# Kernel tuning notes

Measured on AMD Instinct MI355X. Metric: run time of the kernel, lower is better.

## Reference

```python
import jax, jax.numpy as jnp
import numpy as np

EMBED_DIM = 1024
N_HEAD = 16
HEAD_DIM = EMBED_DIM // N_HEAD


def setup_inputs() -> dict:
    key = jax.random.key(0)
    k1, k2, k3 = jax.random.split(key, 3)
    B, S = 2, 2048
    x = jax.random.normal(k1, (B, S, EMBED_DIM), dtype=jnp.float32)
    # kaiming-style scale for the packed QKV projection and output projection
    w_qkv = jax.random.normal(k2, (3 * EMBED_DIM, EMBED_DIM), dtype=jnp.float32) * np.sqrt(2.0 / EMBED_DIM)
    w0 = jax.random.normal(k3, (EMBED_DIM, EMBED_DIM), dtype=jnp.float32) * np.sqrt(2.0 / EMBED_DIM)
    return {"x": x, "w_qkv": w_qkv, "w0": w0}


def reference(x, w_qkv, w0):
    B, S, E = x.shape
    # fused QKV projection (Linear with no bias): x @ w_qkv.T -> [B,S,3E]
    qkv = jnp.einsum('bse,fe->bsf', x, w_qkv)
    q, k, v = jnp.split(qkv, 3, axis=-1)
    # reshape to [B, H, S, D]
    def heads(t):
        return t.reshape(B, S, N_HEAD, HEAD_DIM).transpose(0, 2, 1, 3)
    q, k, v = heads(q), heads(k), heads(v)
    scale = 1.0 / np.sqrt(HEAD_DIM).astype(np.float32)
    scores = jnp.einsum('bhsd,bhtd->bhst', q, k) * scale  # [B,H,S,S]
    # causal additive bias: -inf above the diagonal (same math as the precomputed bias tensor)
    causal = jnp.tril(jnp.ones((S, S), dtype=bool))
    scores = jnp.where(causal, scores, -jnp.inf)
    probs = jax.nn.softmax(scores, axis=-1)
    e = jnp.einsum('bhst,bhtd->bhsd', probs, v)  # [B,H,S,D]
    e = e.transpose(0, 2, 1, 3).reshape(B, S, E)
    # output projection: E @ w0.T
    return jnp.einsum('bse,fe->bsf', e, w0)
```

## Files before the change

### kernel.cpp

```cpp
#include <hip/hip_runtime.h>


typedef unsigned short u16;
typedef short bf16x8 __attribute__((ext_vector_type(8)));
typedef float f32x4 __attribute__((ext_vector_type(4)));
typedef unsigned short u16x4 __attribute__((ext_vector_type(4)));

#define S_LEN 2048
#define EMB 1024
#define NH 16
#define HD 64
#define QKV_W 3072
#define BATCH 2
#define CSC 0.18033688f
#define PSTR 72

static __device__ __forceinline__ u16 f2bf(float f) {
    unsigned x = __float_as_uint(f);
    return (u16)((x + 0x7fffu + ((x >> 16) & 1u)) >> 16);
}

static __device__ __forceinline__ void gld_lds16(const u16* g, u16* l) {
    __builtin_amdgcn_global_load_lds(
        (const __attribute__((address_space(1))) void*)g,
        (__attribute__((address_space(3))) void*)l, 16, 0, 0);
}

#define XN4 (BATCH * S_LEN * EMB / 4)
#define WQ4 (QKV_W * EMB / 4)
#define W04 (EMB * EMB / 4)
__global__ __launch_bounds__(256) void cvt_all(const float* __restrict__ x,
                                               const float* __restrict__ wq,
                                               const float* __restrict__ w0,
                                               u16* __restrict__ xb,
                                               u16* __restrict__ wqb,
                                               u16* __restrict__ w0b) {
    int i = blockIdx.x * 256 + threadIdx.x;
    const float* src;
    u16* dst;
    int off;
    if (i < XN4) { src = x; dst = xb; off = i; }
    else if (i < XN4 + WQ4) { src = wq; dst = wqb; off = i - XN4; }
    else { src = w0; dst = w0b; off = i - XN4 - WQ4; }
    float4 v = ((const float4*)src)[off];
    u16x4 o;
    o[0] = f2bf(v.x); o[1] = f2bf(v.y); o[2] = f2bf(v.z); o[3] = f2bf(v.w);
    ((u16x4*)dst)[off] = o;
}

template <typename OutT, int BN, int BK>
__global__ __launch_bounds__(256) void gemm_bt(const u16* __restrict__ A,
                                               const u16* __restrict__ Bt,
                                               OutT* __restrict__ C,
                                               int M, int N, int K, int qcols) {
    constexpr int NF = BN / 32;
    constexpr int KH = BK / 32;
    constexpr int ACH = 128 * BK / 2048;
    constexpr int BCH = BN * BK / 2048;
    __shared__ alignas(16) u16 As[128 * BK];
    __shared__ alignas(16) u16 Bs[BN * BK];
    const int tid = threadIdx.x;
    const int wave = tid >> 6, lane = tid & 63;
    const int quad = lane >> 4, lr = lane & 15;
    const int m0 = blockIdx.y * 128, n0 = blockIdx.x * BN;
    const int wm = (wave & 1) * 64, wn = (wave >> 1) * (BN / 2);
    const float sc = (n0 < qcols) ? CSC : 1.0f;

    f32x4 acc[4][NF] = {};

    for (int k0 = 0; k0 < K; k0 += BK) {
#pragma unroll
        for (int i = 0; i < ACH; ++i) {
            int chunk = tid + i * 256;
            int row = chunk / (BK / 8);
            int col8 = (chunk % (BK / 8)) * 8;
            gld_lds16(&A[(size_t)(m0 + row) * K + k0 + col8], &As[row * BK + col8]);
        }
#pragma unroll
        for (int i = 0; i < BCH; ++i) {
            int chunk = tid + i * 256;
            int row = chunk / (BK / 8);
            int col8 = (chunk % (BK / 8)) * 8;
            gld_lds16(&Bt[(size_t)(n0 + row) * K + k0 + col8], &Bs[row * BK + col8]);
        }
        __syncthreads();
#pragma unroll
        for (int kh = 0; kh < KH; ++kh) {
            bf16x8 af[4], bf[NF];
#pragma unroll
            for (int i = 0; i < 4; ++i)
                af[i] = *(const bf16x8*)&As[(wm + i * 16 + lr) * BK + kh * 32 + quad * 8];
#pragma unroll
            for (int i = 0; i < NF; ++i)
                bf[i] = *(const bf16x8*)&Bs[(wn + i * 16 + lr) * BK + kh * 32 + quad * 8];
#pragma unroll
            for (int mi = 0; mi < 4; ++mi)
#pragma unroll
                for (int ni = 0; ni < NF; ++ni)
                    acc[mi][ni] = __builtin_amdgcn_mfma_f32_16x16x32_bf16(
                        af[mi], bf[ni], acc[mi][ni], 0, 0, 0);
        }
        __syncthreads();
    }

#pragma unroll
    for (int mi = 0; mi < 4; ++mi) {
#pragma unroll
        for (int r = 0; r < 4; ++r) {
            int gr = m0 + wm + mi * 16 + quad * 4 + r;
#pragma unroll
            for (int ni = 0; ni < NF; ++ni) {
                int gc = n0 + wn + ni * 16 + lr;
                float v = acc[mi][ni][r] * sc;
                if constexpr (sizeof(OutT) == 2)
                    C[(size_t)gr * N + gc] = (OutT)f2bf(v);
                else
                    C[(size_t)gr * N + gc] = (OutT)v;
            }
        }
    }
}

__global__ __launch_bounds__(256) void transpose_v(const u16* __restrict__ qkv,
                                                   u16* __restrict__ vt) {
    __shared__ alignas(16) u16 t[64][72];
    const int s0 = blockIdx.x * 64;
    const int bh = blockIdx.y;
    const int b = bh >> 4, h = bh & 15;
#pragma unroll
    for (int i = 0; i < 2; ++i) {
        int chunk = threadIdx.x + i * 256;
        int row = chunk >> 3;
        int c8 = (chunk & 7) * 8;
        uint4 v = *(const uint4*)&qkv[(size_t)(b * S_LEN + s0 + row) * QKV_W +
                                      2 * EMB + h * HD + c8];
        const u16* p = (const u16*)&v;
#pragma unroll
        for (int jj = 0; jj < 8; ++jj) t[c8 + jj][row] = p[jj];
    }
    __syncthreads();
#pragma unroll
    for (int i = 0; i < 2; ++i) {
        int chunk = threadIdx.x + i * 256;
        int d = chunk >> 3;
        int c8 = (chunk & 7) * 8;
        uint4 v = *(const uint4*)&t[d][c8];
        *(uint4*)&vt[((size_t)bh * HD + d) * S_LEN + s0 + c8] = v;
    }
}

__global__ __launch_bounds__(512, 4) void attn(const u16* __restrict__ qkv,
                                               const u16* __restrict__ vt,
                                               u16* __restrict__ e) {
    const int tid = threadIdx.x;
    const int w = tid >> 6, lane = tid & 63;
    const int quad = lane >> 4, lr = lane & 15;
    const int bx = blockIdx.x, by = blockIdx.y;
    const int flip = (by >> 4) & 1;
    const int pi = flip ? (15 - bx) : bx;
    const int bh = ((by & 15) << 1) | flip;
    const int qtA = pi, qtB = 31 - pi;
    const int b = bh >> 4, h = bh & 15;
    const int myqt = (w < 4) ? qtA : qtB;
    const int qbase = myqt * 64 + (w & 3) * 16;

    __shared__ alignas(16) u16 Ks[2 * 2 * 64 * 32];
    __shared__ alignas(16) u16 Vs[2 * 2 * 64 * 32];
    __shared__ alignas(16) u16 plds[8][16 * PSTR];
    u16* pw = plds[w];

    const u16* qkv_b = qkv + (size_t)b * S_LEN * QKV_W;
    const u16* qrow = qkv_b + (size_t)(qbase + lr) * QKV_W + h * HD + quad * 8;
    const bf16x8 qf0 = *(const bf16x8*)(qrow);
    const bf16x8 qf1 = *(const bf16x8*)(qrow + 32);

    const u16* kbase = qkv_b + EMB + h * HD;
    const u16* vbase = vt + (size_t)bh * HD * S_LEN;

    f32x4 o[4] = {};
    float lsum = 0.f;
    const int qg = qbase + lr;

    const int sr = (w & 3) * 16 + (lane >> 2);
    const int sc = (lane & 3) * 8;

    auto stage = [&](int j, int bb) {
        const int kv0 = j * 64;
        if (w < 4) {
            gld_lds16(kbase + (size_t)(kv0 + sr) * QKV_W + sc,
                      &Ks[bb * 4096 + sr * 32 + sc]);
            gld_lds16(kbase + (size_t)(kv0 + sr) * QKV_W + 32 + sc,
                      &Ks[bb * 4096 + 2048 + sr * 32 + sc]);
        } else {
            gld_lds16(vbase + (size_t)sr * S_LEN + kv0 + sc,
                      &Vs[bb * 4096 + sr * 32 + sc]);
            gld_lds16(vbase + (size_t)sr * S_LEN + kv0 + 32 + sc,
                      &Vs[bb * 4096 + 2048 + sr * 32 + sc]);
        }
    };

    stage(0, 0);
    for (int j = 0; j <= qtB; ++j) {
        const int bb = j & 1;
        __syncthreads();
        if (j < qtB) stage(j + 1, 1 - bb);
        if (j <= myqt) {
            const int kv0 = j * 64;
            const u16* ks = &Ks[bb * 4096];
            const u16* vs = &Vs[bb * 4096];
            f32x4 s[4];
#pragma unroll
            for (int nt = 0; nt < 4; ++nt) {
                bf16x8 k0 = *(const bf16x8*)&ks[(nt * 16 + lr) * 32 + quad * 8];
                bf16x8 k1 = *(const bf16x8*)&ks[2048 + (nt * 16 + lr) * 32 + quad * 8];
                f32x4 z = {};
                z = __builtin_amdgcn_mfma_f32_16x16x32_bf16(k0, qf0, z, 0, 0, 0);
                z = __builtin_amdgcn_mfma_f32_16x16x32_bf16(k1, qf1, z, 0, 0, 0);
                s[nt] = z;
            }
            const bool diag = (j == myqt);
            __builtin_amdgcn_wave_barrier();
#pragma unroll
            for (int nt = 0; nt < 4; ++nt) {
                float p[4];
#pragma unroll
                for (int r = 0; r < 4; ++r) {
                    float pv = exp2f(s[nt][r]);
                    if (diag) pv = (kv0 + nt * 16 + quad * 4 + r > qg) ? 0.f : pv;
                    p[r] = pv;
                }
                lsum += (p[0] + p[1]) + (p[2] + p[3]);
                uint2 pk;
                pk.x = __builtin_amdgcn_perm(__float_as_uint(p[1]),
                                             __float_as_uint(p[0]), 0x07060302u);
                pk.y = __builtin_amdgcn_perm(__float_as_uint(p[3]),
                                             __float_as_uint(p[2]), 0x07060302u);
                *(uint2*)&pw[lr * PSTR + nt * 16 + quad * 4] = pk;
            }
            __builtin_amdgcn_wave_barrier();
            const bf16x8 p0 = *(const bf16x8*)&pw[lr * PSTR + quad * 8];
            const bf16x8 p1 = *(const bf16x8*)&pw[lr * PSTR + 32 + quad * 8];
#pragma unroll
            for (int nt = 0; nt < 4; ++nt) {
                bf16x8 v0 = *(const bf16x8*)&vs[(nt * 16 + lr) * 32 + quad * 8];
                bf16x8 v1 = *(const bf16x8*)&vs[2048 + (nt * 16 + lr) * 32 + quad * 8];
                o[nt] = __builtin_amdgcn_mfma_f32_16x16x32_bf16(p0, v0, o[nt], 0, 0, 0);
                o[nt] = __builtin_amdgcn_mfma_f32_16x16x32_bf16(p1, v1, o[nt], 0, 0, 0);
            }
        }
    }

    float lf = lsum + __shfl_xor(lsum, 16, 64);
    lf += __shfl_xor(lf, 32, 64);
#pragma unroll
    for (int r = 0; r < 4; ++r) {
        float inv = 1.0f / __shfl(lf, quad * 4 + r, 64);
        size_t row = (size_t)(b * S_LEN + qbase + quad * 4 + r) * EMB + h * HD;
#pragma unroll
        for (int nt = 0; nt < 4; ++nt)
            e[row + nt * 16 + lr] = f2bf(o[nt][r] * inv);
    }
}

extern "C" void kernel_launch(void* const* d_in, const int* in_sizes, int n_in,
                              void* d_out, int out_size, void* d_ws, size_t ws_size,
                              hipStream_t stream) {
    const float* x = (const float*)d_in[0];
    const float* w_qkv = (const float*)d_in[1];
    const float* w0 = (const float*)d_in[2];
    float* out = (float*)d_out;

    const size_t M = (size_t)BATCH * S_LEN;
    u16* xb = (u16*)d_ws;
    u16* wqb = xb + M * EMB;
    u16* w0b = wqb + (size_t)QKV_W * EMB;
    u16* qkvb = w0b + (size_t)EMB * EMB;
    u16* vtb = qkvb + M * QKV_W;
    u16* eb = vtb + (size_t)BATCH * NH * HD * S_LEN;

    cvt_all<<<(XN4 + WQ4 + W04) / 256, 256, 0, stream>>>(x, w_qkv, w0, xb, wqb, w0b);

    gemm_bt<u16, 128, 32><<<dim3(QKV_W / 128, M / 128), 256, 0, stream>>>(
        xb, wqb, qkvb, (int)M, QKV_W, EMB, EMB);

    transpose_v<<<dim3(S_LEN / 64, BATCH * NH), 256, 0, stream>>>(qkvb, vtb);

    attn<<<dim3(16, BATCH * NH), 512, 0, stream>>>(qkvb, vtb, eb);

    gemm_bt<float, 64, 64><<<dim3(EMB / 64, M / 128), 256, 0, stream>>>(
        eb, w0b, out, (int)M, EMB, EMB, 0);
}
```

Measured before the change: 189.6 us.

## Fuse V transpose into QKV GEMM epilogue and raise its K tile

The QKV projection GEMM now writes the V columns straight into the transposed [B,H,D,S] layout from its epilogue, which removes the separate transpose_v kernel launch and its extra read and write of V. The QKV GEMM's K tile is also raised from 32 to 64. The transposed stores go to consecutive sequence positions per row (16 lanes hit 16 different d rows), so they are scattered 2-byte writes that may coalesce poorly. The larger K tile doubles shared memory per block.

```diff
diff --git a/kernel.cpp b/kernel.cpp
--- a/kernel.cpp
+++ b/kernel.cpp
@@ -52,6 +52,7 @@
 __global__ __launch_bounds__(256) void gemm_bt(const u16* __restrict__ A,
                                                const u16* __restrict__ Bt,
                                                OutT* __restrict__ C,
+                                               u16* __restrict__ vt,
                                                int M, int N, int K, int qcols) {
     constexpr int NF = BN / 32;
     constexpr int KH = BK / 32;
@@ -103,6 +104,7 @@
         __syncthreads();
     }
 
+    const bool vmode = (vt != nullptr) && (n0 >= 2 * EMB);
 #pragma unroll
     for (int mi = 0; mi < 4; ++mi) {
 #pragma unroll
@@ -112,40 +114,17 @@
             for (int ni = 0; ni < NF; ++ni) {
                 int gc = n0 + wn + ni * 16 + lr;
                 float v = acc[mi][ni][r] * sc;
-                if constexpr (sizeof(OutT) == 2)
+                if (vmode) {
+                    int hd = gc - 2 * EMB;
+                    vt[((size_t)(gr >> 11) * 1024 + hd) * (size_t)S_LEN +
+                       (gr & 2047)] = f2bf(v);
+                } else if constexpr (sizeof(OutT) == 2) {
                     C[(size_t)gr * N + gc] = (OutT)f2bf(v);
-                else
+                } else {
                     C[(size_t)gr * N + gc] = (OutT)v;
-            }
-        }
-    }
-}
-
-__global__ __launch_bounds__(256) void transpose_v(const u16* __restrict__ qkv,
-                                                   u16* __restrict__ vt) {
-    __shared__ alignas(16) u16 t[64][72];
-    const int s0 = blockIdx.x * 64;
-    const int bh = blockIdx.y;
-    const int b = bh >> 4, h = bh & 15;
-#pragma unroll
-    for (int i = 0; i < 2; ++i) {
-        int chunk = threadIdx.x + i * 256;
-        int row = chunk >> 3;
-        int c8 = (chunk & 7) * 8;
-        uint4 v = *(const uint4*)&qkv[(size_t)(b * S_LEN + s0 + row) * QKV_W +
-                                      2 * EMB + h * HD + c8];
-        const u16* p = (const u16*)&v;
-#pragma unroll
-        for (int jj = 0; jj < 8; ++jj) t[c8 + jj][row] = p[jj];
-    }
-    __syncthreads();
-#pragma unroll
-    for (int i = 0; i < 2; ++i) {
-        int chunk = threadIdx.x + i * 256;
-        int d = chunk >> 3;
-        int c8 = (chunk & 7) * 8;
-        uint4 v = *(const uint4*)&t[d][c8];
-        *(uint4*)&vt[((size_t)bh * HD + d) * S_LEN + s0 + c8] = v;
+                }
+            }
+        }
     }
 }
 
@@ -280,13 +259,11 @@
 
     cvt_all<<<(XN4 + WQ4 + W04) / 256, 256, 0, stream>>>(x, w_qkv, w0, xb, wqb, w0b);
 
-    gemm_bt<u16, 128, 32><<<dim3(QKV_W / 128, M / 128), 256, 0, stream>>>(
-        xb, wqb, qkvb, (int)M, QKV_W, EMB, EMB);
-
-    transpose_v<<<dim3(S_LEN / 64, BATCH * NH), 256, 0, stream>>>(qkvb, vtb);
+    gemm_bt<u16, 128, 64><<<dim3(QKV_W / 128, M / 128), 256, 0, stream>>>(
+        xb, wqb, qkvb, vtb, (int)M, QKV_W, EMB, EMB);
 
     attn<<<dim3(16, BATCH * NH), 512, 0, stream>>>(qkvb, vtb, eb);
 
     gemm_bt<float, 64, 64><<<dim3(EMB / 64, M / 128), 256, 0, stream>>>(
-        eb, w0b, out, (int)M, EMB, EMB, 0);
-}
+        eb, w0b, out, nullptr, (int)M, EMB, EMB, 0);
+}
```

After: 213.9 us. +12.8%, slower.
